# Optimization experiments

Measured on AMD Instinct MI355X. Metric: run time of the kernel, lower is better.

Reference implementation:

```python
import jax, jax.numpy as jnp
import numpy as np

B, N, F_IN, D, TOPK, HID = 64, 512, 256, 128, 20, 512


def setup_inputs() -> dict:
    key = jax.random.key(0)
    ks = jax.random.split(key, 10)
    s = lambda fan: 1.0 / np.sqrt(fan)
    return {
        "data": jax.random.normal(ks[0], (B, F_IN, N), jnp.float32),
        "emb_weight": jax.random.normal(ks[1], (N, D), jnp.float32) * s(D),      # nn.Embedding, kaiming-ish
        "lin_w": jax.random.normal(ks[2], (D, F_IN), jnp.float32) * s(F_IN),     # GraphLayer.lin (no bias)
        "att_i": jax.random.normal(ks[3], (D,), jnp.float32) * 0.1,
        "att_j": jax.random.normal(ks[4], (D,), jnp.float32) * 0.1,
        "att_em_i": jax.random.normal(ks[5], (D,), jnp.float32) * 0.1,
        "att_em_j": jax.random.normal(ks[6], (D,), jnp.float32) * 0.1,
        "gnn_bias": jnp.zeros((D,), jnp.float32),
        "bn_gamma": jnp.ones((D,), jnp.float32),
        "bn_beta": jnp.zeros((D,), jnp.float32),
        "w1": jax.random.normal(ks[7], (HID, N), jnp.float32) * s(N),            # Linear(node_num, hidden, bias=False)
        "w2": jax.random.normal(ks[8], (HID, HID), jnp.float32) * s(HID),        # Linear(hidden, hidden)
        "b2": jnp.zeros((HID,), jnp.float32),
    }


def reference(data, emb_weight, lin_w, att_i, att_j, att_em_i, att_em_j,
              gnn_bias, bn_gamma, bn_beta, w1, w2, b2):
    data = jax.lax.stop_gradient(data)                       # x = data.clone().detach()
    b, f_in, n = data.shape
    d = emb_weight.shape[1]
    x = jnp.transpose(data, (0, 2, 1)).reshape(b * n, f_in)  # [B*N, F]

    # --- dynamic graph from detached embedding: cosine topk ---
    W = jax.lax.stop_gradient(emb_weight)
    nrm = jnp.linalg.norm(W, axis=-1)
    cos = (W @ W.T) / (nrm[:, None] * nrm[None, :])
    topk_idx = jax.lax.top_k(cos, TOPK)[1]                   # [N, topk] (learned_graph)
    src = topk_idx.reshape(-1)                               # gated_j (sources)
    dst = jnp.repeat(jnp.arange(n), TOPK)                    # gated_i (destinations)
    offs = (jnp.arange(b) * n)[:, None]
    bsrc = (src[None, :] + offs).reshape(-1)                 # [B*N*topk]
    bdst = (dst[None, :] + offs).reshape(-1)

    # --- GDN GraphLayer (heads=1, concat=False, aggr=add) ---
    xl = x @ lin_w.T                                         # [B*N, D]
    emb_all = jnp.tile(emb_weight, (b, 1))                   # [B*N, D]
    xi, xj = xl[bdst], xl[bsrc]
    ei, ej = emb_all[bdst], emb_all[bsrc]
    alpha = xi @ att_i + ei @ att_em_i + xj @ att_j + ej @ att_em_j   # [E]
    alpha = jax.nn.leaky_relu(alpha, 0.2)
    amax = jax.ops.segment_max(alpha, bdst, num_segments=b * n)
    ex = jnp.exp(alpha - amax[bdst])
    denom = jax.ops.segment_sum(ex, bdst, num_segments=b * n)
    a = ex / denom[bdst]                                     # segment softmax over dest
    agg = jax.ops.segment_sum(xj * a[:, None], bdst, num_segments=b * n) + gnn_bias

    # --- BatchNorm1d (eval: mean 0, var 1) + ReLU ---
    h = agg * (bn_gamma / jnp.sqrt(1.0 + 1e-5)) + bn_beta
    gcn = jax.nn.relu(h).reshape(b, n, d)

    # --- embedding gate + linear block over node dim ---
    out = gcn * emb_weight[None]                             # [B, N, D]
    out = jnp.transpose(out, (0, 2, 1))                      # [B, D, N]
    out = out @ w1.T                                         # [B, D, HID]
    out = out @ w2.T + b2
    out = jax.nn.sigmoid(out)
    return out, emb_weight, topk_idx
```

## Files before the change

kernel.cpp:

```cpp
#include <hip/hip_runtime.h>
#include <hip/hip_bf16.h>

constexpr int B = 64, N = 512, F_IN = 256, D = 128, TOPK = 20, HID = 512;

typedef __attribute__((ext_vector_type(8))) short short8_t;
typedef __attribute__((ext_vector_type(4))) float f32x4;

__device__ inline short f2bs(float f) {
    union { __hip_bfloat16 h; short s; } u; u.h = __float2bfloat16(f); return u.s;
}
__device__ inline float bs2f(short s) {
    return __uint_as_float(((unsigned)(unsigned short)s) << 16);
}

template<int ITERS>
__device__ inline void stage64_bf16(short* ldst, const short* __restrict__ src,
                                    int stride, int k0, int t) {
    #pragma unroll
    for (int i = 0; i < ITERS; ++i) {
        int lin = t + i * 256, row = lin >> 3, seg = lin & 7;
        *(short8_t*)&ldst[row * 72 + seg * 8] =
            *(const short8_t*)&src[(size_t)row * stride + k0 + seg * 8];
    }
}
template<int ITERS>
__device__ inline void stage64_f32(short* ldst, const float* __restrict__ src,
                                   int stride, int k0, int t) {
    #pragma unroll
    for (int i = 0; i < ITERS; ++i) {
        int lin = t + i * 256, row = lin >> 3, seg = lin & 7;
        const float* p = &src[(size_t)row * stride + k0 + seg * 8];
        float4 x = *(const float4*)p, y = *(const float4*)(p + 4);
        short8_t v = { f2bs(x.x), f2bs(x.y), f2bs(x.z), f2bs(x.w),
                       f2bs(y.x), f2bs(y.y), f2bs(y.z), f2bs(y.w) };
        *(short8_t*)&ldst[row * 72 + seg * 8] = v;
    }
}

template<int MS, int NS>
__device__ inline void mfma_tiles64(const short* lds_a, const short* lds_b,
                                    f32x4 (&acc)[MS][NS], int wm, int wn, int lr, int quad) {
    #pragma unroll
    for (int kc = 0; kc < 64; kc += 32) {
        short8_t af[MS], bf[NS];
        #pragma unroll
        for (int ms = 0; ms < MS; ++ms)
            af[ms] = *(const short8_t*)&lds_a[(wm + ms * 16 + lr) * 72 + kc + quad * 8];
        #pragma unroll
        for (int ns = 0; ns < NS; ++ns)
            bf[ns] = *(const short8_t*)&lds_b[(wn + ns * 16 + lr) * 72 + kc + quad * 8];
        #pragma unroll
        for (int ms = 0; ms < MS; ++ms)
            #pragma unroll
            for (int ns = 0; ns < NS; ++ns)
                acc[ms][ns] = __builtin_amdgcn_mfma_f32_16x16x32_bf16(af[ms], bf[ns], acc[ms][ns], 0, 0, 0);
    }
}

__global__ void k_norm(const float* __restrict__ W, const float* __restrict__ aei,
                       const float* __restrict__ aej, float* __restrict__ inv_norm,
                       float* __restrict__ ei, float* __restrict__ ej,
                       float* __restrict__ out_emb) {
    int n = blockIdx.x, t = threadIdx.x;
    float w = W[n * D + t];
    out_emb[n * D + t] = w;
    float s0 = w * w, s1 = w * aei[t], s2 = w * aej[t];
    #pragma unroll
    for (int o = 32; o > 0; o >>= 1) {
        s0 += __shfl_down(s0, o); s1 += __shfl_down(s1, o); s2 += __shfl_down(s2, o);
    }
    __shared__ float r[6];
    if ((t & 63) == 0) { int q = t >> 6; r[q * 3] = s0; r[q * 3 + 1] = s1; r[q * 3 + 2] = s2; }
    __syncthreads();
    if (t == 0) {
        inv_norm[n] = 1.0f / sqrtf(r[0] + r[3]);
        ei[n] = r[1] + r[4];
        ej[n] = r[2] + r[5];
    }
}

__global__ __launch_bounds__(256) void k_cos(const float* __restrict__ W,
                                             const float* __restrict__ inv_norm,
                                             float* __restrict__ cosm) {
    __shared__ float la[32][33];
    __shared__ float lb[32][33];
    int j0 = blockIdx.x * 32, i0 = blockIdx.y * 32, t = threadIdx.x;
    int ix = (t & 15) * 2, jx = (t >> 4) * 2;
    float acc[2][2] = {};
    for (int k0 = 0; k0 < D; k0 += 32) {
        #pragma unroll
        for (int i = 0; i < 4; ++i) {
            int lin = t + i * 256, rl = lin & 31, kk = lin >> 5;
            la[kk][rl] = W[(size_t)(i0 + rl) * D + k0 + kk];
            lb[kk][rl] = W[(size_t)(j0 + rl) * D + k0 + kk];
        }
        __syncthreads();
        #pragma unroll
        for (int kk = 0; kk < 32; ++kk) {
            float a0 = la[kk][ix], a1 = la[kk][ix + 1];
            float b0 = lb[kk][jx], b1 = lb[kk][jx + 1];
            acc[0][0] += a0 * b0; acc[0][1] += a0 * b1;
            acc[1][0] += a1 * b0; acc[1][1] += a1 * b1;
        }
        __syncthreads();
    }
    #pragma unroll
    for (int ii = 0; ii < 2; ++ii) {
        float inv_i = inv_norm[i0 + ix + ii];
        float2 v;
        v.x = acc[ii][0] * inv_i * inv_norm[j0 + jx + 0];
        v.y = acc[ii][1] * inv_i * inv_norm[j0 + jx + 1];
        *(float2*)&cosm[(size_t)(i0 + ix + ii) * N + j0 + jx] = v;
    }
}

__global__ __launch_bounds__(256) void k_sel(const float* __restrict__ cosm,
                                             int* __restrict__ topk,
                                             float* __restrict__ out_idx) {
    int t = threadIdx.x, wid = t >> 6, lane = t & 63;
    int i = blockIdx.x * 4 + wid;
    float4 p0 = *(const float4*)&cosm[(size_t)i * N + lane * 8];
    float4 p1 = *(const float4*)&cosm[(size_t)i * N + lane * 8 + 4];
    float v[8] = {p0.x, p0.y, p0.z, p0.w, p1.x, p1.y, p1.z, p1.w};
    for (int k = 0; k < TOPK; ++k) {
        float bv = v[0]; int bc = 0;
        #pragma unroll
        for (int c = 1; c < 8; ++c) if (v[c] > bv) { bv = v[c]; bc = c; }
        int bj = lane * 8 + bc;
        #pragma unroll
        for (int o = 1; o < 64; o <<= 1) {
            float ov = __shfl_xor(bv, o);
            int  oj = __shfl_xor(bj, o);
            if (ov > bv || (ov == bv && oj < bj)) { bv = ov; bj = oj; }
        }
        if (lane == 0) {
            topk[i * TOPK + k] = bj;
            out_idx[i * TOPK + k] = (float)bj;
        }
        int oc = bj & 7; bool owner = (bj >> 3) == lane;
        #pragma unroll
        for (int c = 0; c < 8; ++c) if (owner && c == oc) v[c] = -INFINITY;
    }
}

__global__ __launch_bounds__(256) void k_xl(const float* __restrict__ data,
                                            const float* __restrict__ lin_w,
                                            const float* __restrict__ att_i,
                                            const float* __restrict__ att_j,
                                            const float* __restrict__ ei,
                                            const float* __restrict__ ej,
                                            short* __restrict__ xlb,
                                            float* __restrict__ s_i,
                                            float* __restrict__ s_j) {
    __shared__ float lt[64][65];
    __shared__ __align__(16) short lds_a[64 * 72];
    __shared__ __align__(16) short lds_b[128 * 72];
    __shared__ float sred[2][64][2];
    int n0 = blockIdx.x * 64, b = blockIdx.y, t = threadIdx.x;
    int wid = t >> 6, lane = t & 63;
    int wm = (wid & 1) * 32, wn = (wid >> 1) * 64;
    int lr = lane & 15, quad = lane >> 4;
    f32x4 acc[2][4] = {};
    for (int k0 = 0; k0 < F_IN; k0 += 64) {
        #pragma unroll
        for (int i = 0; i < 2; ++i) {
            int lin = t + i * 256, f = lin >> 3, ng = (lin & 7) * 8;
            const float* p = &data[((size_t)b * F_IN + k0 + f) * N + n0 + ng];
            float4 v0 = *(const float4*)p, v1 = *(const float4*)(p + 4);
            float* q = &lt[f][ng];
            q[0] = v0.x; q[1] = v0.y; q[2] = v0.z; q[3] = v0.w;
            q[4] = v1.x; q[5] = v1.y; q[6] = v1.z; q[7] = v1.w;
        }
        stage64_f32<4>(lds_b, lin_w, F_IN, k0, t);
        __syncthreads();
        #pragma unroll
        for (int i = 0; i < 2; ++i) {
            int lin = t + i * 256, row = lin >> 3, seg = lin & 7;
            short8_t a;
            #pragma unroll
            for (int j = 0; j < 8; ++j) a[j] = f2bs(lt[seg * 8 + j][row]);
            *(short8_t*)&lds_a[row * 72 + seg * 8] = a;
        }
        __syncthreads();
        mfma_tiles64<2, 4>(lds_a, lds_b, acc, wm, wn, lr, quad);
        __syncthreads();
    }
    #pragma unroll
    for (int ms = 0; ms < 2; ++ms)
        #pragma unroll
        for (int ns = 0; ns < 4; ++ns) {
            int mb = wm + ms * 16 + quad * 4, col = wn + ns * 16 + lr;
            #pragma unroll
            for (int r = 0; r < 4; ++r)
                xlb[((size_t)b * N + n0 + mb + r) * D + col] = f2bs(acc[ms][ns][r]);
        }
    float si8[8], sj8[8];
    #pragma unroll
    for (int ms = 0; ms < 2; ++ms)
        #pragma unroll
        for (int r = 0; r < 4; ++r) {
            float si = 0.f, sj = 0.f;
            #pragma unroll
            for (int ns = 0; ns < 4; ++ns) {
                int col = wn + ns * 16 + lr;
                float x = acc[ms][ns][r];
                si += x * att_i[col];
                sj += x * att_j[col];
            }
            si8[ms * 4 + r] = si; sj8[ms * 4 + r] = sj;
        }
    #pragma unroll
    for (int o = 1; o < 16; o <<= 1) {
        #pragma unroll
        for (int i = 0; i < 8; ++i) {
            si8[i] += __shfl_xor(si8[i], o);
            sj8[i] += __shfl_xor(sj8[i], o);
        }
    }
    if (lr == 0) {
        #pragma unroll
        for (int ms = 0; ms < 2; ++ms)
            #pragma unroll
            for (int r = 0; r < 4; ++r) {
                int row = wm + ms * 16 + quad * 4 + r;
                sred[wid >> 1][row][0] = si8[ms * 4 + r];
                sred[wid >> 1][row][1] = sj8[ms * 4 + r];
            }
    }
    __syncthreads();
    if (t < 64) {
        int n = n0 + t;
        s_i[b * N + n] = sred[0][t][0] + sred[1][t][0] + ei[n];
        s_j[b * N + n] = sred[0][t][1] + sred[1][t][1] + ej[n];
    }
}

__global__ __launch_bounds__(256) void k_attn2(const short* __restrict__ xlb,
                                               const float* __restrict__ emb,
                                               const int* __restrict__ topk,
                                               const float* __restrict__ s_i,
                                               const float* __restrict__ s_j,
                                               const float* __restrict__ gnn_bias,
                                               const float* __restrict__ bn_gamma,
                                               const float* __restrict__ bn_beta,
                                               short* __restrict__ Gt) {
    __shared__ float alph[16][20];
    __shared__ int   js[16][20];
    __shared__ float lt[16][129];
    int n0 = blockIdx.x * 16, b = blockIdx.y, t = threadIdx.x;
    for (int e = t; e < 16 * TOPK; e += 256) {
        int nl = e / TOPK, k = e - nl * TOPK;
        int j = topk[(n0 + nl) * TOPK + k];
        js[nl][k] = j;
        float al = s_i[b * N + n0 + nl] + s_j[b * N + j];
        alph[nl][k] = al >= 0.f ? al : 0.2f * al;
    }
    __syncthreads();
    if (t < 16) {
        float m = -INFINITY;
        for (int k = 0; k < TOPK; ++k) m = fmaxf(m, alph[t][k]);
        float s = 0.f;
        for (int k = 0; k < TOPK; ++k) { float e_ = expf(alph[t][k] - m); alph[t][k] = e_; s += e_; }
        float inv = 1.0f / s;
        for (int k = 0; k < TOPK; ++k) alph[t][k] *= inv;
    }
    __syncthreads();
    {
        int nl = t >> 4, dl = (t & 15) * 8;
        float a[8] = {};
        for (int k = 0; k < TOPK; ++k) {
            float w = alph[nl][k];
            short8_t xv = *(const short8_t*)&xlb[((size_t)b * N + js[nl][k]) * D + dl];
            #pragma unroll
            for (int c = 0; c < 8; ++c) a[c] += w * bs2f(xv[c]);
        }
        const float bnk = 0.9999950000374997f;
        #pragma unroll
        for (int c = 0; c < 8; ++c) {
            int d = dl + c;
            float h = (a[c] + gnn_bias[d]) * (bn_gamma[d] * bnk) + bn_beta[d];
            h = fmaxf(h, 0.f);
            lt[nl][d] = h * emb[(n0 + nl) * D + d];
        }
    }
    __syncthreads();
    {
        int d = t >> 1, half = t & 1;
        short8_t v;
        #pragma unroll
        for (int j = 0; j < 8; ++j) v[j] = f2bs(lt[half * 8 + j][d]);
        *(short8_t*)&Gt[((size_t)b * D + d) * N + n0 + half * 8] = v;
    }
}

__global__ __launch_bounds__(256) void k_gemm1(const short* __restrict__ Gt,
                                               const float* __restrict__ w1,
                                               short* __restrict__ out1) {
    __shared__ __align__(16) short lds_a[64 * 72];
    __shared__ __align__(16) short lds_b[64 * 72];
    int h0 = blockIdx.x * 64, d0 = blockIdx.y * 64, b = blockIdx.z, t = threadIdx.x;
    int wid = t >> 6, lane = t & 63;
    int wm = (wid >> 1) * 32, wn = (wid & 1) * 32;
    int lr = lane & 15, quad = lane >> 4;
    f32x4 acc[2][2] = {};
    const short* Asrc = Gt + ((size_t)b * D + d0) * N;
    const float* Bsrc = w1 + (size_t)h0 * N;
    for (int k0 = 0; k0 < N; k0 += 64) {
        stage64_bf16<2>(lds_a, Asrc, N, k0, t);
        stage64_f32<2>(lds_b, Bsrc, N, k0, t);
        __syncthreads();
        mfma_tiles64<2, 2>(lds_a, lds_b, acc, wm, wn, lr, quad);
        __syncthreads();
    }
    #pragma unroll
    for (int ms = 0; ms < 2; ++ms)
        #pragma unroll
        for (int ns = 0; ns < 2; ++ns) {
            int mb = d0 + wm + ms * 16 + quad * 4, col = h0 + wn + ns * 16 + lr;
            #pragma unroll
            for (int r = 0; r < 4; ++r)
                out1[((size_t)b * D + mb + r) * HID + col] = f2bs(acc[ms][ns][r]);
        }
}

__global__ __launch_bounds__(256) void k_gemm2(const short* __restrict__ out1,
                                               const float* __restrict__ w2,
                                               const float* __restrict__ b2,
                                               float* __restrict__ out) {
    __shared__ __align__(16) short lds_a[64 * 72];
    __shared__ __align__(16) short lds_b[64 * 72];
    int h0 = blockIdx.x * 64, d0 = blockIdx.y * 64, b = blockIdx.z, t = threadIdx.x;
    int wid = t >> 6, lane = t & 63;
    int wm = (wid >> 1) * 32, wn = (wid & 1) * 32;
    int lr = lane & 15, quad = lane >> 4;
    f32x4 acc[2][2] = {};
    const short* Asrc = out1 + ((size_t)b * D + d0) * HID;
    const float* Bsrc = w2 + (size_t)h0 * HID;
    for (int k0 = 0; k0 < HID; k0 += 64) {
        stage64_bf16<2>(lds_a, Asrc, HID, k0, t);
        stage64_f32<2>(lds_b, Bsrc, HID, k0, t);
        __syncthreads();
        mfma_tiles64<2, 2>(lds_a, lds_b, acc, wm, wn, lr, quad);
        __syncthreads();
    }
    #pragma unroll
    for (int ms = 0; ms < 2; ++ms)
        #pragma unroll
        for (int ns = 0; ns < 2; ++ns) {
            int mb = d0 + wm + ms * 16 + quad * 4, col = h0 + wn + ns * 16 + lr;
            float bias = b2[col];
            #pragma unroll
            for (int r = 0; r < 4; ++r)
                out[((size_t)b * D + mb + r) * HID + col] =
                    1.0f / (1.0f + expf(-(acc[ms][ns][r] + bias)));
        }
}

extern "C" void kernel_launch(void* const* d_in, const int* in_sizes, int n_in,
                              void* d_out, int out_size, void* d_ws, size_t ws_size,
                              hipStream_t stream) {
    const float* data     = (const float*)d_in[0];
    const float* emb      = (const float*)d_in[1];
    const float* lin_w    = (const float*)d_in[2];
    const float* att_i    = (const float*)d_in[3];
    const float* att_j    = (const float*)d_in[4];
    const float* att_em_i = (const float*)d_in[5];
    const float* att_em_j = (const float*)d_in[6];
    const float* gnn_bias = (const float*)d_in[7];
    const float* bn_gamma = (const float*)d_in[8];
    const float* bn_beta  = (const float*)d_in[9];
    const float* w1       = (const float*)d_in[10];
    const float* w2       = (const float*)d_in[11];
    const float* b2       = (const float*)d_in[12];
    float* out            = (float*)d_out;

    float* ws       = (float*)d_ws;
    float* inv_norm = ws;
    float* ei       = ws + 512;
    float* ej       = ws + 1024;
    int*   topk     = (int*)(ws + 1536);
    float* s_i      = ws + 1536 + N * TOPK;
    float* s_j      = s_i + B * N;
    short* S        = (short*)(ws + 77312);
    short* Gt       = S;
    short* out1     = S + (size_t)B * D * N;
    short* xlb      = S + 2 * (size_t)B * D * N;
    float* cosm     = (float*)S;

    float* out_emb = out + (size_t)B * D * HID;
    float* out_idx = out_emb + (size_t)N * D;

    hipLaunchKernelGGL(k_norm,  dim3(N),              dim3(D),   0, stream, emb, att_em_i, att_em_j, inv_norm, ei, ej, out_emb);
    hipLaunchKernelGGL(k_cos,   dim3(N / 32, N / 32), dim3(256), 0, stream, emb, inv_norm, cosm);
    hipLaunchKernelGGL(k_sel,   dim3(N / 4),          dim3(256), 0, stream, cosm, topk, out_idx);
    hipLaunchKernelGGL(k_xl,    dim3(N / 64, B),      dim3(256), 0, stream, data, lin_w, att_i, att_j, ei, ej, xlb, s_i, s_j);
    hipLaunchKernelGGL(k_attn2, dim3(N / 16, B),      dim3(256), 0, stream, xlb, emb, topk, s_i, s_j, gnn_bias, bn_gamma, bn_beta, Gt);
    hipLaunchKernelGGL(k_gemm1, dim3(HID / 64, D / 64, B), dim3(256), 0, stream, Gt, w1, out1);
    hipLaunchKernelGGL(k_gemm2, dim3(HID / 64, D / 64, B), dim3(256), 0, stream, out1, w2, b2, out);
}
```

Baseline: 189.2 us.

## Fuse attention aggregation and both node-dim GEMMs into one kernel

Replaces k_attn2, k_gemm1 and k_gemm2 with a single kernel, launched with 256 blocks, that does the aggregation for a 32-channel slice of one batch and keeps the G and intermediate tiles in LDS. This removes the global round trips for Gt and out1 and two launches. In exchange, w1 and w2 are read straight from global memory as fp32 and converted to bf16 inside the MFMA loop, with no LDS staging or reuse. The grid is also much smaller, so occupancy and weight bandwidth may limit it.

Result: slower. 224.5 us (+18.7%).

```diff
diff --git a/kernel.cpp b/kernel.cpp
--- a/kernel.cpp
+++ b/kernel.cpp
@@ -13,16 +13,6 @@
     return __uint_as_float(((unsigned)(unsigned short)s) << 16);
 }
 
-template<int ITERS>
-__device__ inline void stage64_bf16(short* ldst, const short* __restrict__ src,
-                                    int stride, int k0, int t) {
-    #pragma unroll
-    for (int i = 0; i < ITERS; ++i) {
-        int lin = t + i * 256, row = lin >> 3, seg = lin & 7;
-        *(short8_t*)&ldst[row * 72 + seg * 8] =
-            *(const short8_t*)&src[(size_t)row * stride + k0 + seg * 8];
-    }
-}
 template<int ITERS>
 __device__ inline void stage64_f32(short* ldst, const float* __restrict__ src,
                                    int stride, int k0, int t) {
@@ -235,125 +225,119 @@
     }
 }
 
-__global__ __launch_bounds__(256) void k_attn2(const short* __restrict__ xlb,
-                                               const float* __restrict__ emb,
-                                               const int* __restrict__ topk,
-                                               const float* __restrict__ s_i,
-                                               const float* __restrict__ s_j,
-                                               const float* __restrict__ gnn_bias,
-                                               const float* __restrict__ bn_gamma,
-                                               const float* __restrict__ bn_beta,
-                                               short* __restrict__ Gt) {
-    __shared__ float alph[16][20];
-    __shared__ int   js[16][20];
-    __shared__ float lt[16][129];
-    int n0 = blockIdx.x * 16, b = blockIdx.y, t = threadIdx.x;
-    for (int e = t; e < 16 * TOPK; e += 256) {
-        int nl = e / TOPK, k = e - nl * TOPK;
-        int j = topk[(n0 + nl) * TOPK + k];
-        js[nl][k] = j;
-        float al = s_i[b * N + n0 + nl] + s_j[b * N + j];
-        alph[nl][k] = al >= 0.f ? al : 0.2f * al;
-    }
-    __syncthreads();
-    if (t < 16) {
+__global__ __launch_bounds__(256) void k_mega(const short* __restrict__ xlb,
+                                              const float* __restrict__ emb,
+                                              const int* __restrict__ topk,
+                                              const float* __restrict__ s_i,
+                                              const float* __restrict__ s_j,
+                                              const float* __restrict__ gnn_bias,
+                                              const float* __restrict__ bn_gamma,
+                                              const float* __restrict__ bn_beta,
+                                              const float* __restrict__ w1,
+                                              const float* __restrict__ w2,
+                                              const float* __restrict__ b2,
+                                              float* __restrict__ out) {
+    __shared__ float s_ij[2][N];
+    __shared__ __align__(16) short G[32 * 520];
+    __shared__ __align__(16) short O1[32 * 520];
+    int d0 = blockIdx.x * 32, b = blockIdx.y, t = threadIdx.x;
+    int wv = t >> 6, lane = t & 63, lr = lane & 15, quad = lane >> 4;
+
+    s_ij[0][t] = s_i[b * N + t];      s_ij[0][t + 256] = s_i[b * N + t + 256];
+    s_ij[1][t] = s_j[b * N + t];      s_ij[1][t + 256] = s_j[b * N + t + 256];
+    __syncthreads();
+
+    const float bnk = 0.9999950000374997f;
+    for (int p = 0; p < 8; ++p) {
+        int n = p * 64 + (t >> 2), g = t & 3;
+        int js[TOPK]; float a[TOPK];
+        #pragma unroll
+        for (int k = 0; k < TOPK; ++k) js[k] = topk[n * TOPK + k];
+        float siv = s_ij[0][n];
+        #pragma unroll
+        for (int k = 0; k < TOPK; ++k) {
+            float al = siv + s_ij[1][js[k]];
+            a[k] = al >= 0.f ? al : 0.2f * al;
+        }
         float m = -INFINITY;
-        for (int k = 0; k < TOPK; ++k) m = fmaxf(m, alph[t][k]);
+        #pragma unroll
+        for (int k = 0; k < TOPK; ++k) m = fmaxf(m, a[k]);
         float s = 0.f;
-        for (int k = 0; k < TOPK; ++k) { float e_ = expf(alph[t][k] - m); alph[t][k] = e_; s += e_; }
+        #pragma unroll
+        for (int k = 0; k < TOPK; ++k) { a[k] = expf(a[k] - m); s += a[k]; }
         float inv = 1.0f / s;
-        for (int k = 0; k < TOPK; ++k) alph[t][k] *= inv;
-    }
-    __syncthreads();
+        float acc[8] = {};
+        #pragma unroll 4
+        for (int k = 0; k < TOPK; ++k) {
+            float wgt = a[k] * inv;
+            short8_t xv = *(const short8_t*)&xlb[((size_t)b * N + js[k]) * D + d0 + g * 8];
+            #pragma unroll
+            for (int c = 0; c < 8; ++c) acc[c] += wgt * bs2f(xv[c]);
+        }
+        #pragma unroll
+        for (int c = 0; c < 8; ++c) {
+            int d = d0 + g * 8 + c;
+            float h = (acc[c] + gnn_bias[d]) * (bn_gamma[d] * bnk) + bn_beta[d];
+            h = fmaxf(h, 0.f);
+            G[(g * 8 + c) * 520 + n] = f2bs(h * emb[(size_t)n * D + d]);
+        }
+    }
+    __syncthreads();
+
     {
-        int nl = t >> 4, dl = (t & 15) * 8;
-        float a[8] = {};
-        for (int k = 0; k < TOPK; ++k) {
-            float w = alph[nl][k];
-            short8_t xv = *(const short8_t*)&xlb[((size_t)b * N + js[nl][k]) * D + dl];
-            #pragma unroll
-            for (int c = 0; c < 8; ++c) a[c] += w * bs2f(xv[c]);
-        }
-        const float bnk = 0.9999950000374997f;
-        #pragma unroll
-        for (int c = 0; c < 8; ++c) {
-            int d = dl + c;
-            float h = (a[c] + gnn_bias[d]) * (bn_gamma[d] * bnk) + bn_beta[d];
-            h = fmaxf(h, 0.f);
-            lt[nl][d] = h * emb[(n0 + nl) * D + d];
-        }
-    }
-    __syncthreads();
+        f32x4 acc1[2][8] = {};
+        for (int c = 0; c < 16; ++c) {
+            short8_t af0 = *(const short8_t*)&G[lr * 520 + c * 32 + quad * 8];
+            short8_t af1 = *(const short8_t*)&G[(16 + lr) * 520 + c * 32 + quad * 8];
+            #pragma unroll
+            for (int ht = 0; ht < 8; ++ht) {
+                const float* wp = &w1[(size_t)(wv * 128 + ht * 16 + lr) * N + c * 32 + quad * 8];
+                float4 p0 = *(const float4*)wp, p1 = *(const float4*)(wp + 4);
+                short8_t bf = { f2bs(p0.x), f2bs(p0.y), f2bs(p0.z), f2bs(p0.w),
+                                f2bs(p1.x), f2bs(p1.y), f2bs(p1.z), f2bs(p1.w) };
+                acc1[0][ht] = __builtin_amdgcn_mfma_f32_16x16x32_bf16(af0, bf, acc1[0][ht], 0, 0, 0);
+                acc1[1][ht] = __builtin_amdgcn_mfma_f32_16x16x32_bf16(af1, bf, acc1[1][ht], 0, 0, 0);
+            }
+        }
+        #pragma unroll
+        for (int ms = 0; ms < 2; ++ms)
+            #pragma unroll
+            for (int ht = 0; ht < 8; ++ht)
+                #pragma unroll
+                for (int r = 0; r < 4; ++r)
+                    O1[(ms * 16 + quad * 4 + r) * 520 + wv * 128 + ht * 16 + lr] = f2bs(acc1[ms][ht][r]);
+    }
+    __syncthreads();
+
     {
-        int d = t >> 1, half = t & 1;
-        short8_t v;
-        #pragma unroll
-        for (int j = 0; j < 8; ++j) v[j] = f2bs(lt[half * 8 + j][d]);
-        *(short8_t*)&Gt[((size_t)b * D + d) * N + n0 + half * 8] = v;
-    }
-}
-
-__global__ __launch_bounds__(256) void k_gemm1(const short* __restrict__ Gt,
-                                               const float* __restrict__ w1,
-                                               short* __restrict__ out1) {
-    __shared__ __align__(16) short lds_a[64 * 72];
-    __shared__ __align__(16) short lds_b[64 * 72];
-    int h0 = blockIdx.x * 64, d0 = blockIdx.y * 64, b = blockIdx.z, t = threadIdx.x;
-    int wid = t >> 6, lane = t & 63;
-    int wm = (wid >> 1) * 32, wn = (wid & 1) * 32;
-    int lr = lane & 15, quad = lane >> 4;
-    f32x4 acc[2][2] = {};
-    const short* Asrc = Gt + ((size_t)b * D + d0) * N;
-    const float* Bsrc = w1 + (size_t)h0 * N;
-    for (int k0 = 0; k0 < N; k0 += 64) {
-        stage64_bf16<2>(lds_a, Asrc, N, k0, t);
-        stage64_f32<2>(lds_b, Bsrc, N, k0, t);
-        __syncthreads();
-        mfma_tiles64<2, 2>(lds_a, lds_b, acc, wm, wn, lr, quad);
-        __syncthreads();
-    }
-    #pragma unroll
-    for (int ms = 0; ms < 2; ++ms)
-        #pragma unroll
-        for (int ns = 0; ns < 2; ++ns) {
-            int mb = d0 + wm + ms * 16 + quad * 4, col = h0 + wn + ns * 16 + lr;
-            #pragma unroll
-            for (int r = 0; r < 4; ++r)
-                out1[((size_t)b * D + mb + r) * HID + col] = f2bs(acc[ms][ns][r]);
-        }
-}
-
-__global__ __launch_bounds__(256) void k_gemm2(const short* __restrict__ out1,
-                                               const float* __restrict__ w2,
-                                               const float* __restrict__ b2,
-                                               float* __restrict__ out) {
-    __shared__ __align__(16) short lds_a[64 * 72];
-    __shared__ __align__(16) short lds_b[64 * 72];
-    int h0 = blockIdx.x * 64, d0 = blockIdx.y * 64, b = blockIdx.z, t = threadIdx.x;
-    int wid = t >> 6, lane = t & 63;
-    int wm = (wid >> 1) * 32, wn = (wid & 1) * 32;
-    int lr = lane & 15, quad = lane >> 4;
-    f32x4 acc[2][2] = {};
-    const short* Asrc = out1 + ((size_t)b * D + d0) * HID;
-    const float* Bsrc = w2 + (size_t)h0 * HID;
-    for (int k0 = 0; k0 < HID; k0 += 64) {
-        stage64_bf16<2>(lds_a, Asrc, HID, k0, t);
-        stage64_f32<2>(lds_b, Bsrc, HID, k0, t);
-        __syncthreads();
-        mfma_tiles64<2, 2>(lds_a, lds_b, acc, wm, wn, lr, quad);
-        __syncthreads();
-    }
-    #pragma unroll
-    for (int ms = 0; ms < 2; ++ms)
-        #pragma unroll
-        for (int ns = 0; ns < 2; ++ns) {
-            int mb = d0 + wm + ms * 16 + quad * 4, col = h0 + wn + ns * 16 + lr;
-            float bias = b2[col];
-            #pragma unroll
-            for (int r = 0; r < 4; ++r)
-                out[((size_t)b * D + mb + r) * HID + col] =
-                    1.0f / (1.0f + expf(-(acc[ms][ns][r] + bias)));
-        }
+        f32x4 acc2[2][8] = {};
+        for (int c = 0; c < 16; ++c) {
+            short8_t af0 = *(const short8_t*)&O1[lr * 520 + c * 32 + quad * 8];
+            short8_t af1 = *(const short8_t*)&O1[(16 + lr) * 520 + c * 32 + quad * 8];
+            #pragma unroll
+            for (int ht = 0; ht < 8; ++ht) {
+                const float* wp = &w2[(size_t)(wv * 128 + ht * 16 + lr) * HID + c * 32 + quad * 8];
+                float4 p0 = *(const float4*)wp, p1 = *(const float4*)(wp + 4);
+                short8_t bf = { f2bs(p0.x), f2bs(p0.y), f2bs(p0.z), f2bs(p0.w),
+                                f2bs(p1.x), f2bs(p1.y), f2bs(p1.z), f2bs(p1.w) };
+                acc2[0][ht] = __builtin_amdgcn_mfma_f32_16x16x32_bf16(af0, bf, acc2[0][ht], 0, 0, 0);
+                acc2[1][ht] = __builtin_amdgcn_mfma_f32_16x16x32_bf16(af1, bf, acc2[1][ht], 0, 0, 0);
+            }
+        }
+        #pragma unroll
+        for (int ms = 0; ms < 2; ++ms)
+            #pragma unroll
+            for (int ht = 0; ht < 8; ++ht) {
+                int h2 = wv * 128 + ht * 16 + lr;
+                float bias = b2[h2];
+                #pragma unroll
+                for (int r = 0; r < 4; ++r) {
+                    int d = d0 + ms * 16 + quad * 4 + r;
+                    out[((size_t)b * D + d) * HID + h2] =
+                        1.0f / (1.0f + expf(-(acc2[ms][ht][r] + bias)));
+                }
+            }
+    }
 }
 
 extern "C" void kernel_launch(void* const* d_in, const int* in_sizes, int n_in,
@@ -382,19 +366,15 @@
     float* s_i      = ws + 1536 + N * TOPK;
     float* s_j      = s_i + B * N;
     short* S        = (short*)(ws + 77312);
-    short* Gt       = S;
-    short* out1     = S + (size_t)B * D * N;
+    float* cosm     = (float*)S;
     short* xlb      = S + 2 * (size_t)B * D * N;
-    float* cosm     = (float*)S;
 
     float* out_emb = out + (size_t)B * D * HID;
     float* out_idx = out_emb + (size_t)N * D;
 
-    hipLaunchKernelGGL(k_norm,  dim3(N),              dim3(D),   0, stream, emb, att_em_i, att_em_j, inv_norm, ei, ej, out_emb);
-    hipLaunchKernelGGL(k_cos,   dim3(N / 32, N / 32), dim3(256), 0, stream, emb, inv_norm, cosm);
-    hipLaunchKernelGGL(k_sel,   dim3(N / 4),          dim3(256), 0, stream, cosm, topk, out_idx);
-    hipLaunchKernelGGL(k_xl,    dim3(N / 64, B),      dim3(256), 0, stream, data, lin_w, att_i, att_j, ei, ej, xlb, s_i, s_j);
-    hipLaunchKernelGGL(k_attn2, dim3(N / 16, B),      dim3(256), 0, stream, xlb, emb, topk, s_i, s_j, gnn_bias, bn_gamma, bn_beta, Gt);
-    hipLaunchKernelGGL(k_gemm1, dim3(HID / 64, D / 64, B), dim3(256), 0, stream, Gt, w1, out1);
-    hipLaunchKernelGGL(k_gemm2, dim3(HID / 64, D / 64, B), dim3(256), 0, stream, out1, w2, b2, out);
-}
+    hipLaunchKernelGGL(k_norm, dim3(N),              dim3(D),   0, stream, emb, att_em_i, att_em_j, inv_norm, ei, ej, out_emb);
+    hipLaunchKernelGGL(k_cos,  dim3(N / 32, N / 32), dim3(256), 0, stream, emb, inv_norm, cosm);
+    hipLaunchKernelGGL(k_sel,  dim3(N / 4),          dim3(256), 0, stream, cosm, topk, out_idx);
+    hipLaunchKernelGGL(k_xl,   dim3(N / 64, B),      dim3(256), 0, stream, data, lin_w, att_i, att_j, ei, ej, xlb, s_i, s_j);
+    hipLaunchKernelGGL(k_mega, dim3(D / 32, B),      dim3(256), 0, stream, xlb, emb, topk, s_i, s_j, gnn_bias, bn_gamma, bn_beta, w1, w2, b2, out);
+}
```

## Pre-convert weights to bf16 once and halve k_xl node tile

Applied to the files above, without the earlier changes.

Adds a small kernel that converts lin_w, w1 and w2 to bf16 once per call, so the GEMM kernels stage bf16 weights directly instead of reloading fp32 and converting in every block. This cuts global read traffic and conversion ALU work in k_xl, k_gemm1 and k_gemm2, at the cost of one extra launch and a workspace region. Separately, k_xl now tiles 32 nodes per block instead of 64, doubling the grid for more parallelism. In exchange, each block reloads the weight tile for half as many rows.

New measurement: 182.7 us. 3.4% less time.

```diff
diff --git a/kernel.cpp b/kernel.cpp
--- a/kernel.cpp
+++ b/kernel.cpp
@@ -23,19 +23,6 @@
             *(const short8_t*)&src[(size_t)row * stride + k0 + seg * 8];
     }
 }
-template<int ITERS>
-__device__ inline void stage64_f32(short* ldst, const float* __restrict__ src,
-                                   int stride, int k0, int t) {
-    #pragma unroll
-    for (int i = 0; i < ITERS; ++i) {
-        int lin = t + i * 256, row = lin >> 3, seg = lin & 7;
-        const float* p = &src[(size_t)row * stride + k0 + seg * 8];
-        float4 x = *(const float4*)p, y = *(const float4*)(p + 4);
-        short8_t v = { f2bs(x.x), f2bs(x.y), f2bs(x.z), f2bs(x.w),
-                       f2bs(y.x), f2bs(y.y), f2bs(y.z), f2bs(y.w) };
-        *(short8_t*)&ldst[row * 72 + seg * 8] = v;
-    }
-}
 
 template<int MS, int NS>
 __device__ inline void mfma_tiles64(const short* lds_a, const short* lds_b,
@@ -55,6 +42,24 @@
             for (int ns = 0; ns < NS; ++ns)
                 acc[ms][ns] = __builtin_amdgcn_mfma_f32_16x16x32_bf16(af[ms], bf[ns], acc[ms][ns], 0, 0, 0);
     }
+}
+
+__global__ __launch_bounds__(256) void k_wcvt(const float* __restrict__ lin_w,
+                                              const float* __restrict__ w1,
+                                              const float* __restrict__ w2,
+                                              short* __restrict__ lin_wb,
+                                              short* __restrict__ w1b,
+                                              short* __restrict__ w2b) {
+    int bid = blockIdx.x, t = threadIdx.x;
+    const float* src; short* dst; int base;
+    if (bid < 16)       { src = lin_w; dst = lin_wb; base = bid * 2048; }
+    else if (bid < 144) { src = w1;    dst = w1b;    base = (bid - 16) * 2048; }
+    else                { src = w2;    dst = w2b;    base = (bid - 144) * 2048; }
+    int idx = base + t * 8;
+    float4 x = *(const float4*)(src + idx), y = *(const float4*)(src + idx + 4);
+    short8_t v = { f2bs(x.x), f2bs(x.y), f2bs(x.z), f2bs(x.w),
+                   f2bs(y.x), f2bs(y.y), f2bs(y.z), f2bs(y.w) };
+    *(short8_t*)(dst + idx) = v;
 }
 
 __global__ void k_norm(const float* __restrict__ W, const float* __restrict__ aei,
@@ -144,7 +149,7 @@
 }
 
 __global__ __launch_bounds__(256) void k_xl(const float* __restrict__ data,
-                                            const float* __restrict__ lin_w,
+                                            const short* __restrict__ lin_wb,
                                             const float* __restrict__ att_i,
                                             const float* __restrict__ att_j,
                                             const float* __restrict__ ei,
@@ -152,83 +157,75 @@
                                             short* __restrict__ xlb,
                                             float* __restrict__ s_i,
                                             float* __restrict__ s_j) {
-    __shared__ float lt[64][65];
-    __shared__ __align__(16) short lds_a[64 * 72];
+    __shared__ float lt[64][33];
+    __shared__ __align__(16) short lds_a[32 * 72];
     __shared__ __align__(16) short lds_b[128 * 72];
-    __shared__ float sred[2][64][2];
-    int n0 = blockIdx.x * 64, b = blockIdx.y, t = threadIdx.x;
+    __shared__ float sred[2][32][2];
+    int n0 = blockIdx.x * 32, b = blockIdx.y, t = threadIdx.x;
     int wid = t >> 6, lane = t & 63;
-    int wm = (wid & 1) * 32, wn = (wid >> 1) * 64;
+    int wm = (wid & 1) * 16, wn = (wid >> 1) * 64;
     int lr = lane & 15, quad = lane >> 4;
-    f32x4 acc[2][4] = {};
+    f32x4 acc[1][4] = {};
     for (int k0 = 0; k0 < F_IN; k0 += 64) {
-        #pragma unroll
-        for (int i = 0; i < 2; ++i) {
-            int lin = t + i * 256, f = lin >> 3, ng = (lin & 7) * 8;
+        {
+            int f = t >> 2, ng = (t & 3) * 8;
             const float* p = &data[((size_t)b * F_IN + k0 + f) * N + n0 + ng];
             float4 v0 = *(const float4*)p, v1 = *(const float4*)(p + 4);
             float* q = &lt[f][ng];
             q[0] = v0.x; q[1] = v0.y; q[2] = v0.z; q[3] = v0.w;
             q[4] = v1.x; q[5] = v1.y; q[6] = v1.z; q[7] = v1.w;
         }
-        stage64_f32<4>(lds_b, lin_w, F_IN, k0, t);
-        __syncthreads();
-        #pragma unroll
-        for (int i = 0; i < 2; ++i) {
-            int lin = t + i * 256, row = lin >> 3, seg = lin & 7;
+        stage64_bf16<4>(lds_b, lin_wb, F_IN, k0, t);
+        __syncthreads();
+        {
+            int row = t >> 3, seg = t & 7;
             short8_t a;
             #pragma unroll
             for (int j = 0; j < 8; ++j) a[j] = f2bs(lt[seg * 8 + j][row]);
             *(short8_t*)&lds_a[row * 72 + seg * 8] = a;
         }
         __syncthreads();
-        mfma_tiles64<2, 4>(lds_a, lds_b, acc, wm, wn, lr, quad);
-        __syncthreads();
-    }
-    #pragma unroll
-    for (int ms = 0; ms < 2; ++ms)
+        mfma_tiles64<1, 4>(lds_a, lds_b, acc, wm, wn, lr, quad);
+        __syncthreads();
+    }
+    #pragma unroll
+    for (int ns = 0; ns < 4; ++ns) {
+        int mb = wm + quad * 4, col = wn + ns * 16 + lr;
+        #pragma unroll
+        for (int r = 0; r < 4; ++r)
+            xlb[((size_t)b * N + n0 + mb + r) * D + col] = f2bs(acc[0][ns][r]);
+    }
+    float si4[4], sj4[4];
+    #pragma unroll
+    for (int r = 0; r < 4; ++r) {
+        float si = 0.f, sj = 0.f;
         #pragma unroll
         for (int ns = 0; ns < 4; ++ns) {
-            int mb = wm + ms * 16 + quad * 4, col = wn + ns * 16 + lr;
-            #pragma unroll
-            for (int r = 0; r < 4; ++r)
-                xlb[((size_t)b * N + n0 + mb + r) * D + col] = f2bs(acc[ms][ns][r]);
-        }
-    float si8[8], sj8[8];
-    #pragma unroll
-    for (int ms = 0; ms < 2; ++ms)
+            int col = wn + ns * 16 + lr;
+            float x = acc[0][ns][r];
+            si += x * att_i[col];
+            sj += x * att_j[col];
+        }
+        si4[r] = si; sj4[r] = sj;
+    }
+    #pragma unroll
+    for (int o = 1; o < 16; o <<= 1) {
+        #pragma unroll
+        for (int i = 0; i < 4; ++i) {
+            si4[i] += __shfl_xor(si4[i], o);
+            sj4[i] += __shfl_xor(sj4[i], o);
+        }
+    }
+    if (lr == 0) {
         #pragma unroll
         for (int r = 0; r < 4; ++r) {
-            float si = 0.f, sj = 0.f;
-            #pragma unroll
-            for (int ns = 0; ns < 4; ++ns) {
-                int col = wn + ns * 16 + lr;
-                float x = acc[ms][ns][r];
-                si += x * att_i[col];
-                sj += x * att_j[col];
-            }
-            si8[ms * 4 + r] = si; sj8[ms * 4 + r] = sj;
-        }
-    #pragma unroll
-    for (int o = 1; o < 16; o <<= 1) {
-        #pragma unroll
-        for (int i = 0; i < 8; ++i) {
-            si8[i] += __shfl_xor(si8[i], o);
-            sj8[i] += __shfl_xor(sj8[i], o);
-        }
-    }
-    if (lr == 0) {
-        #pragma unroll
-        for (int ms = 0; ms < 2; ++ms)
-            #pragma unroll
-            for (int r = 0; r < 4; ++r) {
-                int row = wm + ms * 16 + quad * 4 + r;
-                sred[wid >> 1][row][0] = si8[ms * 4 + r];
-                sred[wid >> 1][row][1] = sj8[ms * 4 + r];
-            }
+            int row = wm + quad * 4 + r;
+            sred[wid >> 1][row][0] = si4[r];
+            sred[wid >> 1][row][1] = sj4[r];
+        }
     }
     __syncthreads();
-    if (t < 64) {
+    if (t < 32) {
         int n = n0 + t;
         s_i[b * N + n] = sred[0][t][0] + sred[1][t][0] + ei[n];
         s_j[b * N + n] = sred[0][t][1] + sred[1][t][1] + ej[n];
@@ -294,7 +291,7 @@
 }
 
 __global__ __launch_bounds__(256) void k_gemm1(const short* __restrict__ Gt,
-                                               const float* __restrict__ w1,
+                                               const short* __restrict__ w1b,
                                                short* __restrict__ out1) {
     __shared__ __align__(16) short lds_a[64 * 72];
     __shared__ __align__(16) short lds_b[64 * 72];
@@ -304,10 +301,10 @@
     int lr = lane & 15, quad = lane >> 4;
     f32x4 acc[2][2] = {};
     const short* Asrc = Gt + ((size_t)b * D + d0) * N;
-    const float* Bsrc = w1 + (size_t)h0 * N;
+    const short* Bsrc = w1b + (size_t)h0 * N;
     for (int k0 = 0; k0 < N; k0 += 64) {
         stage64_bf16<2>(lds_a, Asrc, N, k0, t);
-        stage64_f32<2>(lds_b, Bsrc, N, k0, t);
+        stage64_bf16<2>(lds_b, Bsrc, N, k0, t);
         __syncthreads();
         mfma_tiles64<2, 2>(lds_a, lds_b, acc, wm, wn, lr, quad);
         __syncthreads();
@@ -324,7 +321,7 @@
 }
 
 __global__ __launch_bounds__(256) void k_gemm2(const short* __restrict__ out1,
-                                               const float* __restrict__ w2,
+                                               const short* __restrict__ w2b,
                                                const float* __restrict__ b2,
                                                float* __restrict__ out) {
     __shared__ __align__(16) short lds_a[64 * 72];
@@ -335,10 +332,10 @@
     int lr = lane & 15, quad = lane >> 4;
     f32x4 acc[2][2] = {};
     const short* Asrc = out1 + ((size_t)b * D + d0) * HID;
-    const float* Bsrc = w2 + (size_t)h0 * HID;
+    const short* Bsrc = w2b + (size_t)h0 * HID;
     for (int k0 = 0; k0 < HID; k0 += 64) {
         stage64_bf16<2>(lds_a, Asrc, HID, k0, t);
-        stage64_f32<2>(lds_b, Bsrc, HID, k0, t);
+        stage64_bf16<2>(lds_b, Bsrc, HID, k0, t);
         __syncthreads();
         mfma_tiles64<2, 2>(lds_a, lds_b, acc, wm, wn, lr, quad);
         __syncthreads();
@@ -381,7 +378,10 @@
     int*   topk     = (int*)(ws + 1536);
     float* s_i      = ws + 1536 + N * TOPK;
     float* s_j      = s_i + B * N;
-    short* S        = (short*)(ws + 77312);
+    short* lin_wb   = (short*)(ws + 77312);
+    short* w1b      = lin_wb + D * F_IN;
+    short* w2b      = w1b + HID * N;
+    short* S        = w2b + HID * HID;
     short* Gt       = S;
     short* out1     = S + (size_t)B * D * N;
     short* xlb      = S + 2 * (size_t)B * D * N;
@@ -390,11 +390,12 @@
     float* out_emb = out + (size_t)B * D * HID;
     float* out_idx = out_emb + (size_t)N * D;
 
+    hipLaunchKernelGGL(k_wcvt,  dim3(272),            dim3(256), 0, stream, lin_w, w1, w2, lin_wb, w1b, w2b);
     hipLaunchKernelGGL(k_norm,  dim3(N),              dim3(D),   0, stream, emb, att_em_i, att_em_j, inv_norm, ei, ej, out_emb);
     hipLaunchKernelGGL(k_cos,   dim3(N / 32, N / 32), dim3(256), 0, stream, emb, inv_norm, cosm);
     hipLaunchKernelGGL(k_sel,   dim3(N / 4),          dim3(256), 0, stream, cosm, topk, out_idx);
-    hipLaunchKernelGGL(k_xl,    dim3(N / 64, B),      dim3(256), 0, stream, data, lin_w, att_i, att_j, ei, ej, xlb, s_i, s_j);
+    hipLaunchKernelGGL(k_xl,    dim3(N / 32, B),      dim3(256), 0, stream, data, lin_wb, att_i, att_j, ei, ej, xlb, s_i, s_j);
     hipLaunchKernelGGL(k_attn2, dim3(N / 16, B),      dim3(256), 0, stream, xlb, emb, topk, s_i, s_j, gnn_bias, bn_gamma, bn_beta, Gt);
-    hipLaunchKernelGGL(k_gemm1, dim3(HID / 64, D / 64, B), dim3(256), 0, stream, Gt, w1, out1);
-    hipLaunchKernelGGL(k_gemm2, dim3(HID / 64, D / 64, B), dim3(256), 0, stream, out1, w2, b2, out);
-}
+    hipLaunchKernelGGL(k_gemm1, dim3(HID / 64, D / 64, B), dim3(256), 0, stream, Gt, w1b, out1);
+    hipLaunchKernelGGL(k_gemm2, dim3(HID / 64, D / 64, B), dim3(256), 0, stream, out1, w2b, b2, out);
+}
```
